# Kernel tuning notes

Measured on AMD Instinct MI355X. Metric: run time of the kernel, lower is better.

The kernel has to match this reference:

```python
import jax, jax.numpy as jnp
import numpy as np

N = 100000      # nodes
E = 1200000     # edges (avg degree ~12)
F_IN = 64       # input feature dim
HID = 64        # hidden_channels
OUT = 64        # out_channels


def setup_inputs() -> dict:
    key = jax.random.key(0)
    ks = jax.random.split(key, 9)
    s_in = 1.0 / np.sqrt(F_IN)
    s_h = 1.0 / np.sqrt(HID)
    inp = {
        "x": jax.random.normal(ks[0], (N, F_IN), dtype=jnp.float32),
        "edge_index": jax.random.randint(ks[1], (2, E), 0, N, dtype=jnp.int64),
        # conv_in: lin_l (with bias) applied to aggregated msgs, lin_r (no bias) to self
        "Wl_in": jax.random.normal(ks[2], (HID, F_IN), dtype=jnp.float32) * s_in,
        "bl_in": jnp.zeros((HID,), dtype=jnp.float32),
        "Wr_in": jax.random.normal(ks[3], (HID, F_IN), dtype=jnp.float32) * s_in,
        # conv_med (shared across the 2 middle applications)
        "Wl_med": jax.random.normal(ks[4], (HID, HID), dtype=jnp.float32) * s_h,
        "bl_med": jnp.zeros((HID,), dtype=jnp.float32),
        "Wr_med": jax.random.normal(ks[5], (HID, HID), dtype=jnp.float32) * s_h,
        # conv_out
        "Wl_out": jax.random.normal(ks[6], (OUT, HID), dtype=jnp.float32) * s_h,
        "bl_out": jnp.zeros((OUT,), dtype=jnp.float32),
        "Wr_out": jax.random.normal(ks[7], (OUT, HID), dtype=jnp.float32) * s_h,
    }
    return inp


def reference(x, edge_index, Wl_in, bl_in, Wr_in, Wl_med, bl_med, Wr_med,
              Wl_out, bl_out, Wr_out):
    src = edge_index[0]
    dst = edge_index[1]
    n = x.shape[0]

    def sage(h, Wl, bl, Wr):
        # sum-aggregate neighbor messages h_j into each destination node i
        agg = jax.ops.segment_sum(h[src], dst, num_segments=n)  # [N, F]
        return agg @ Wl.T + bl + h @ Wr.T

    # eval mode: dropout is identity
    h = jnp.tanh(sage(x, Wl_in, bl_in, Wr_in))
    for _ in range(2):  # conv_med applied twice with shared weights
        h = jnp.tanh(sage(h, Wl_med, bl_med, Wr_med))
    return sage(h, Wl_out, bl_out, Wr_out)
```

## Files before the change

### kernel.cpp

```cpp
#include <hip/hip_runtime.h>
#include <cstdint>

#define F 64
#define TILE1 8192
#define MAXFB 1024
#define SCAN_BLK 1024
#define ECAP 2048

typedef short bf16x8 __attribute__((ext_vector_type(8)));
typedef float f32x4  __attribute__((ext_vector_type(4)));

__device__ __forceinline__ unsigned short f2b(float f) {
    unsigned u = __float_as_uint(f);
    unsigned r = u + 0x7fffu + ((u >> 16) & 1u);
    return (unsigned short)(r >> 16);
}
__device__ __forceinline__ void add8(float* a, uint4 u) {
    const unsigned* p = (const unsigned*)&u;
#pragma unroll
    for (int i = 0; i < 4; ++i) {
        a[2 * i + 0] += __uint_as_float(p[i] << 16);
        a[2 * i + 1] += __uint_as_float(p[i] & 0xffff0000u);
    }
}

__global__ __launch_bounds__(256) void prep_hist_kernel(
    const float* __restrict__ Wl0, const float* __restrict__ Wr0,
    const float* __restrict__ Wl1, const float* __restrict__ Wr1,
    const float* __restrict__ Wl2, const float* __restrict__ Wr2,
    ushort* __restrict__ wbuf,
    const float* __restrict__ x, ushort* __restrict__ xb, int nElem,
    const int* __restrict__ dst, int* __restrict__ binMat,
    int E, int NB1, int nf) {
    __shared__ int h[MAXFB];
    int b = blockIdx.x;
    int t = threadIdx.x;
    if (b < 12) {
        int g = b * 256 + t;
        int set = g >> 10;
        int fl = g & 1023;
        int f = fl >> 6;
        int l = fl & 63;
        int s = f >> 2;
        int ot = f & 3;
        const float* Wl = (set == 0) ? Wl0 : (set == 1) ? Wl1 : Wl2;
        const float* Wr = (set == 0) ? Wr0 : (set == 1) ? Wr1 : Wr2;
        int o = ot * 16 + (l & 15);
        int k0 = s * 32 + (l >> 4) * 8;
        unsigned d[4];
#pragma unroll
        for (int p = 0; p < 4; ++p) {
            int ka = k0 + 2 * p, kb = k0 + 2 * p + 1;
            float va = (ka < 64) ? Wl[o * 64 + ka] : Wr[o * 64 + (ka - 64)];
            float vb = (kb < 64) ? Wl[o * 64 + kb] : Wr[o * 64 + (kb - 64)];
            d[p] = (unsigned)f2b(va) | ((unsigned)f2b(vb) << 16);
        }
        ((uint4*)wbuf)[g] = make_uint4(d[0], d[1], d[2], d[3]);
    } else if (b < 12 + NB1) {
        int tb = b - 12;
        for (int i = t; i < nf; i += 256) h[i] = 0;
        __syncthreads();
        int base = tb * TILE1;
        int end = min(base + TILE1, E);
        const int4* d4 = (const int4*)dst;
        int n4 = (end - base) >> 2;
        int b4 = base >> 2;
        for (int k = t; k < n4; k += 256) {
            int4 v = d4[b4 + k];
            atomicAdd(&h[v.x >> 7], 1);
            atomicAdd(&h[v.y >> 7], 1);
            atomicAdd(&h[v.z >> 7], 1);
            atomicAdd(&h[v.w >> 7], 1);
        }
        __syncthreads();
        for (int i = t; i < nf; i += 256) binMat[i * NB1 + tb] = h[i];
    } else {
        int i = (b - 12 - NB1) * 256 + t;
        int n4 = nElem >> 2;
        if (i < n4) {
            float4 v = ((const float4*)x)[i];
            uint2 o;
            o.x = (unsigned)f2b(v.x) | ((unsigned)f2b(v.y) << 16);
            o.y = (unsigned)f2b(v.z) | ((unsigned)f2b(v.w) << 16);
            ((uint2*)xb)[i] = o;
        }
    }
}

__global__ __launch_bounds__(SCAN_BLK) void scan_blocks_kernel(
    int* __restrict__ a, int* __restrict__ blockSums, int len) {
    __shared__ int sh[SCAN_BLK];
    int t = threadIdx.x;
    int i = blockIdx.x * SCAN_BLK + t;
    int v = (i < len) ? a[i] : 0;
    sh[t] = v;
    __syncthreads();
    for (int off = 1; off < SCAN_BLK; off <<= 1) {
        int add = (t >= off) ? sh[t - off] : 0;
        __syncthreads();
        sh[t] += add;
        __syncthreads();
    }
    int incl = sh[t];
    if (i < len) a[i] = incl - v;
    if (t == SCAN_BLK - 1) blockSums[blockIdx.x] = incl;
}

__device__ __forceinline__ void scan_sums_lds(
    const int* __restrict__ blockSums, int nbScan, int* sBS) {
    int t = threadIdx.x;
    int v = (t < nbScan) ? blockSums[t] : 0;
    sBS[t] = v;
    __syncthreads();
    for (int off = 1; off < 256; off <<= 1) {
        int add = (t >= off) ? sBS[t - off] : 0;
        __syncthreads();
        sBS[t] += add;
        __syncthreads();
    }
    int excl = sBS[t] - v;
    __syncthreads();
    sBS[t] = excl;
    __syncthreads();
}

__global__ __launch_bounds__(256) void scatter_kernel(
    const int* __restrict__ src, const int* __restrict__ dst,
    const int* __restrict__ binMat, const int* __restrict__ blockSums,
    unsigned* __restrict__ stage2, int E, int NB1, int nf, int nbScan) {
    __shared__ int cur[MAXFB];
    __shared__ int sBS[256];
    int t = threadIdx.x;
    scan_sums_lds(blockSums, nbScan, sBS);
    for (int i = t; i < nf; i += 256) {
        int j = i * NB1 + blockIdx.x;
        cur[i] = binMat[j] + sBS[j >> 10];
    }
    __syncthreads();
    int base = blockIdx.x * TILE1;
    int end = min(base + TILE1, E);
    const int4* s4 = (const int4*)src;
    const int4* d4 = (const int4*)dst;
    int n4 = (end - base) >> 2;
    int b4 = base >> 2;
    for (int k = t; k < n4; k += 256) {
        int4 s = s4[b4 + k];
        int4 d = d4[b4 + k];
        int p0 = atomicAdd(&cur[d.x >> 7], 1);
        int p1 = atomicAdd(&cur[d.y >> 7], 1);
        int p2 = atomicAdd(&cur[d.z >> 7], 1);
        int p3 = atomicAdd(&cur[d.w >> 7], 1);
        stage2[p0] = ((unsigned)(d.x & 127) << 17) | (unsigned)s.x;
        stage2[p1] = ((unsigned)(d.y & 127) << 17) | (unsigned)s.y;
        stage2[p2] = ((unsigned)(d.z & 127) << 17) | (unsigned)s.z;
        stage2[p3] = ((unsigned)(d.w & 127) << 17) | (unsigned)s.w;
    }
}

__global__ __launch_bounds__(256) void phase2_kernel(
    const unsigned* __restrict__ stage2, const int* __restrict__ binMat,
    const int* __restrict__ blockSums,
    int* __restrict__ csrSrc, int* __restrict__ rowStart,
    int* __restrict__ perm,
    int E, int NB1, int nf, int nbScan) {
    __shared__ int cnt[128];
    __shared__ int pre[129];
    __shared__ int cur[128];
    __shared__ int sBS[256];
    __shared__ int permL[128];
    int b = blockIdx.x;
    int t = threadIdx.x;
    scan_sums_lds(blockSums, nbScan, sBS);
    int j0 = b * NB1;
    int s = binMat[j0] + sBS[j0 >> 10];
    int e2 = E;
    if (b + 1 < nf) {
        int j1 = (b + 1) * NB1;
        e2 = binMat[j1] + sBS[j1 >> 10];
    }
    if (t < 128) cnt[t] = 0;
    __syncthreads();
    for (int i = s + t; i < e2; i += 256)
        atomicAdd(&cnt[(stage2[i] >> 17) & 127], 1);
    __syncthreads();
    if (t < 128) pre[t + 1] = cnt[t];
    if (t == 0) pre[0] = 0;
    if (t < 128) {
        int my = cnt[t];
        int r = 0;
        for (int j = 0; j < 128; ++j) {
            int cj = cnt[j];
            r += (cj > my) || (cj == my && j < t);
        }
        permL[r] = t;
    }
    __syncthreads();
    for (int off = 1; off < 128; off <<= 1) {
        int v = 0;
        if (t < 128 && (t + 1) > off) v = pre[t + 1 - off];
        __syncthreads();
        if (t < 128 && (t + 1) > off) pre[t + 1] += v;
        __syncthreads();
    }
    if (t < 128) cur[t] = pre[t];
    if (t < 129) rowStart[b * 128 + t] = s + pre[t];
    if (t < 128) perm[b * 128 + t] = permL[t];
    __syncthreads();
    for (int i = s + t; i < e2; i += 256) {
        unsigned w = stage2[i];
        int pos = atomicAdd(&cur[(w >> 17) & 127], 1);
        csrSrc[s + pos] = (int)(w & 0x1FFFFu);
    }
}

__global__ __launch_bounds__(512, 4) void fused_layer(
    const ushort* __restrict__ hb, const int* __restrict__ rowStart,
    const int* __restrict__ csrSrc, const int* __restrict__ perm,
    const ushort* __restrict__ wbuf,
    const float* __restrict__ bl, void* __restrict__ out, int n, int flags) {
    __shared__ __align__(16) ushort smem[128 * 72];
    __shared__ int eidx[ECAP];

    int t = threadIdx.x;
    int node0b = blockIdx.x * 128;
    const uint4* h16 = (const uint4*)hb;

    int e0 = rowStart[node0b];
    int ne = rowStart[node0b + 128] - e0;
    bool useL = (ne <= ECAP);
    if (useL) {
        for (int i = t; i < ne; i += 512) eidx[i] = csrSrc[e0 + i];
    }
    __syncthreads();

    {
        int c = t & 7;
        int tm = t >> 3;
        const int* permB = perm + blockIdx.x * 128;
        int nl0 = permB[tm];
        int nl1 = permB[127 - tm];

        auto run = [&](auto IDX) {
#pragma unroll 1
            for (int r = 0; r < 2; ++r) {
                int nl = (r == 0) ? nl0 : nl1;
                int node = node0b + nl;
                float a[8] = {0.f, 0.f, 0.f, 0.f, 0.f, 0.f, 0.f, 0.f};
                int e = rowStart[node];
                int end = rowStart[node + 1];
                for (; e + 3 < end; e += 4) {
                    int s0 = IDX(e + 0);
                    int s1 = IDX(e + 1);
                    int s2 = IDX(e + 2);
                    int s3 = IDX(e + 3);
                    uint4 u0 = h16[(size_t)s0 * 8 + c];
                    uint4 u1 = h16[(size_t)s1 * 8 + c];
                    uint4 u2 = h16[(size_t)s2 * 8 + c];
                    uint4 u3 = h16[(size_t)s3 * 8 + c];
                    add8(a, u0); add8(a, u1); add8(a, u2); add8(a, u3);
                }
                for (; e < end; ++e) {
                    uint4 u0 = h16[(size_t)IDX(e) * 8 + c];
                    add8(a, u0);
                }
                unsigned d[4];
#pragma unroll
                for (int p = 0; p < 4; ++p)
                    d[p] = (unsigned)f2b(a[2 * p]) | ((unsigned)f2b(a[2 * p + 1]) << 16);
                *(uint4*)(smem + nl * 72 + c * 8) = make_uint4(d[0], d[1], d[2], d[3]);
            }
        };
        if (useL) run([&](int e) { return eidx[e - e0]; });
        else      run([&](int e) { return csrSrc[e]; });
    }
    __syncthreads();

    int w = t >> 6;
    int l = t & 63;
    int quad = l >> 4;
    int lo = l & 15;

    f32x4 acc[4];
#pragma unroll
    for (int ot = 0; ot < 4; ++ot) {
        float bv = bl[ot * 16 + lo];
        f32x4 bvv = {bv, bv, bv, bv};
        acc[ot] = bvv;
    }

#pragma unroll
    for (int s = 0; s < 4; ++s) {
        bf16x8 A;
        if (s < 2) {
            int nl = w * 16 + lo;
            A = *(const bf16x8*)(smem + nl * 72 + s * 32 + quad * 8);
        } else {
            size_t node = (size_t)node0b + w * 16 + lo;
            A = *(const bf16x8*)(hb + node * 64 + (s & 1) * 32 + quad * 8);
        }
#pragma unroll
        for (int ot = 0; ot < 4; ++ot) {
            bf16x8 B = *(const bf16x8*)(wbuf + (((s * 4 + ot) * 64) + l) * 8);
            acc[ot] = __builtin_amdgcn_mfma_f32_16x16x32_bf16(A, B, acc[ot], 0, 0, 0);
        }
    }
    __syncthreads();

    float* outT = (float*)smem;
    int whalf = w >> 2;
    int wrow = (w & 3) * 16;

#pragma unroll
    for (int half = 0; half < 2; ++half) {
        if (whalf == half) {
#pragma unroll
            for (int ot = 0; ot < 4; ++ot) {
                f32x4 v = acc[ot];
                if (flags & 1) {
                    v[0] = tanhf(v[0]); v[1] = tanhf(v[1]);
                    v[2] = tanhf(v[2]); v[3] = tanhf(v[3]);
                }
                int row = wrow + quad * 4;
                int col = ot * 16 + lo;
#pragma unroll
                for (int r = 0; r < 4; ++r)
                    outT[(row + r) * 68 + col] = v[r];
            }
        }
        __syncthreads();
        int hr = t >> 3;
        int node = node0b + half * 64 + hr;
        if (node < n) {
            const float* srcp = &outT[hr * 68 + (t & 7) * 8];
            if (flags & 2) {
                uint4* o8 = (uint4*)out;
                unsigned dd[4];
#pragma unroll
                for (int p = 0; p < 4; ++p) {
                    float va = srcp[2 * p];
                    float vb = srcp[2 * p + 1];
                    dd[p] = (unsigned)f2b(va) | ((unsigned)f2b(vb) << 16);
                }
                o8[(size_t)node * 8 + (t & 7)] = make_uint4(dd[0], dd[1], dd[2], dd[3]);
            } else {
                float4* o16 = (float4*)out;
#pragma unroll
                for (int q = 0; q < 2; ++q) {
                    float4 v = *(const float4*)(srcp + q * 4);
                    o16[(size_t)node * 16 + (t & 7) * 2 + q] = v;
                }
            }
        }
        if (half == 0) __syncthreads();
    }
}

extern "C" void kernel_launch(void* const* d_in, const int* in_sizes, int n_in,
                              void* d_out, int out_size, void* d_ws, size_t ws_size,
                              hipStream_t stream) {
    const float* x      = (const float*)d_in[0];
    const int*   edges  = (const int*)d_in[1];
    const float* Wl_in  = (const float*)d_in[2];
    const float* bl_in  = (const float*)d_in[3];
    const float* Wr_in  = (const float*)d_in[4];
    const float* Wl_med = (const float*)d_in[5];
    const float* bl_med = (const float*)d_in[6];
    const float* Wr_med = (const float*)d_in[7];
    const float* Wl_out = (const float*)d_in[8];
    const float* bl_out = (const float*)d_in[9];
    const float* Wr_out = (const float*)d_in[10];

    const int N = in_sizes[0] / F;
    const int E = in_sizes[1] / 2;
    const int* src = edges;
    const int* dst = edges + E;

    const int nf  = (N + 127) >> 7;
    const int NB1 = (E + TILE1 - 1) / TILE1;
    const int NR  = nf * 128;
    const int scanLen = nf * NB1;
    const int nbScan = (scanLen + SCAN_BLK - 1) / SCAN_BLK;

    ushort*  wbuf      = (ushort*)d_ws;
    ushort*  xb        = wbuf + 3 * 8192;
    ushort*  hAb       = xb + (size_t)NR * F;
    ushort*  hBb       = hAb + (size_t)NR * F;
    int*     rowStart  = (int*)(hBb + (size_t)NR * F);
    int*     blockSums = rowStart + NR + 2;
    int*     binMat    = blockSums + SCAN_BLK;
    unsigned* stage2   = (unsigned*)(binMat + scanLen);
    int*     csrSrc    = (int*)(stage2 + E);
    int*     perm      = csrSrc + E;

    const int prep_blocks = 12 + NB1 + (N * F / 4 + 255) / 256;

    prep_hist_kernel<<<prep_blocks, 256, 0, stream>>>(
        Wl_in, Wr_in, Wl_med, Wr_med, Wl_out, Wr_out, wbuf, x, xb, N * F,
        dst, binMat, E, NB1, nf);
    scan_blocks_kernel<<<nbScan, SCAN_BLK, 0, stream>>>(binMat, blockSums, scanLen);
    scatter_kernel<<<NB1, 256, 0, stream>>>(src, dst, binMat, blockSums, stage2, E, NB1, nf, nbScan);
    phase2_kernel<<<nf, 256, 0, stream>>>(stage2, binMat, blockSums, csrSrc, rowStart, perm, E, NB1, nf, nbScan);

    fused_layer<<<nf, 512, 0, stream>>>(xb,  rowStart, csrSrc, perm, wbuf,         bl_in,  hAb,   N, 3);
    fused_layer<<<nf, 512, 0, stream>>>(hAb, rowStart, csrSrc, perm, wbuf + 8192,  bl_med, hBb,   N, 3);
    fused_layer<<<nf, 512, 0, stream>>>(hBb, rowStart, csrSrc, perm, wbuf + 8192,  bl_med, hAb,   N, 3);
    fused_layer<<<nf, 512, 0, stream>>>(hAb, rowStart, csrSrc, perm, wbuf + 16384, bl_out, d_out, N, 0);
}
```

Baseline: 256.9 us.

## Use 1024-thread blocks: one node per thread group, split MFMA output tiles across waves

The fused SAGE layer kernel now launches 1024 threads per block instead of 512. Each 8-thread group gathers exactly one node rather than two, and the node-to-group mapping uses a strided rank over the degree-sorted permutation to spread load across waves. In the matmul stage, 16 waves each compute two of the four output column tiles, and the store phase uses 16 threads per row. This aims for more memory-level parallelism in the gather, at the cost of fewer resident blocks per CU and more per-block synchronisation.

```diff
diff --git a/kernel.cpp b/kernel.cpp
--- a/kernel.cpp
+++ b/kernel.cpp
@@ -213,7 +213,7 @@
     }
 }
 
-__global__ __launch_bounds__(512, 4) void fused_layer(
+__global__ __launch_bounds__(1024, 2) void fused_layer(
     const ushort* __restrict__ hb, const int* __restrict__ rowStart,
     const int* __restrict__ csrSrc, const int* __restrict__ perm,
     const ushort* __restrict__ wbuf,
@@ -229,126 +229,118 @@
     int ne = rowStart[node0b + 128] - e0;
     bool useL = (ne <= ECAP);
     if (useL) {
-        for (int i = t; i < ne; i += 512) eidx[i] = csrSrc[e0 + i];
+        for (int i = t; i < ne; i += 1024) eidx[i] = csrSrc[e0 + i];
     }
     __syncthreads();
 
     {
         int c = t & 7;
         int tm = t >> 3;
-        const int* permB = perm + blockIdx.x * 128;
-        int nl0 = permB[tm];
-        int nl1 = permB[127 - tm];
+        int rank = ((tm & 7) << 4) + (tm >> 3);
+        int nl = perm[blockIdx.x * 128 + rank];
+        int node = node0b + nl;
+        float a[8] = {0.f, 0.f, 0.f, 0.f, 0.f, 0.f, 0.f, 0.f};
+        int e = rowStart[node];
+        int end = rowStart[node + 1];
 
         auto run = [&](auto IDX) {
-#pragma unroll 1
-            for (int r = 0; r < 2; ++r) {
-                int nl = (r == 0) ? nl0 : nl1;
-                int node = node0b + nl;
-                float a[8] = {0.f, 0.f, 0.f, 0.f, 0.f, 0.f, 0.f, 0.f};
-                int e = rowStart[node];
-                int end = rowStart[node + 1];
-                for (; e + 3 < end; e += 4) {
-                    int s0 = IDX(e + 0);
-                    int s1 = IDX(e + 1);
-                    int s2 = IDX(e + 2);
-                    int s3 = IDX(e + 3);
-                    uint4 u0 = h16[(size_t)s0 * 8 + c];
-                    uint4 u1 = h16[(size_t)s1 * 8 + c];
-                    uint4 u2 = h16[(size_t)s2 * 8 + c];
-                    uint4 u3 = h16[(size_t)s3 * 8 + c];
-                    add8(a, u0); add8(a, u1); add8(a, u2); add8(a, u3);
-                }
-                for (; e < end; ++e) {
-                    uint4 u0 = h16[(size_t)IDX(e) * 8 + c];
-                    add8(a, u0);
-                }
-                unsigned d[4];
-#pragma unroll
-                for (int p = 0; p < 4; ++p)
-                    d[p] = (unsigned)f2b(a[2 * p]) | ((unsigned)f2b(a[2 * p + 1]) << 16);
-                *(uint4*)(smem + nl * 72 + c * 8) = make_uint4(d[0], d[1], d[2], d[3]);
+            for (; e + 3 < end; e += 4) {
+                int s0 = IDX(e + 0);
+                int s1 = IDX(e + 1);
+                int s2 = IDX(e + 2);
+                int s3 = IDX(e + 3);
+                uint4 u0 = h16[(size_t)s0 * 8 + c];
+                uint4 u1 = h16[(size_t)s1 * 8 + c];
+                uint4 u2 = h16[(size_t)s2 * 8 + c];
+                uint4 u3 = h16[(size_t)s3 * 8 + c];
+                add8(a, u0); add8(a, u1); add8(a, u2); add8(a, u3);
+            }
+            for (; e < end; ++e) {
+                uint4 u0 = h16[(size_t)IDX(e) * 8 + c];
+                add8(a, u0);
             }
         };
-        if (useL) run([&](int e) { return eidx[e - e0]; });
-        else      run([&](int e) { return csrSrc[e]; });
+        if (useL) run([&](int ei) { return eidx[ei - e0]; });
+        else      run([&](int ei) { return csrSrc[ei]; });
+
+        unsigned d[4];
+#pragma unroll
+        for (int p = 0; p < 4; ++p)
+            d[p] = (unsigned)f2b(a[2 * p]) | ((unsigned)f2b(a[2 * p + 1]) << 16);
+        *(uint4*)(smem + nl * 72 + c * 8) = make_uint4(d[0], d[1], d[2], d[3]);
     }
     __syncthreads();
 
     int w = t >> 6;
+    int m = w & 7;
+    int oth = w >> 3;
     int l = t & 63;
     int quad = l >> 4;
     int lo = l & 15;
 
-    f32x4 acc[4];
-#pragma unroll
-    for (int ot = 0; ot < 4; ++ot) {
-        float bv = bl[ot * 16 + lo];
+    f32x4 acc[2];
+#pragma unroll
+    for (int oi = 0; oi < 2; ++oi) {
+        float bv = bl[(oth * 2 + oi) * 16 + lo];
         f32x4 bvv = {bv, bv, bv, bv};
-        acc[ot] = bvv;
+        acc[oi] = bvv;
     }
 
 #pragma unroll
     for (int s = 0; s < 4; ++s) {
         bf16x8 A;
         if (s < 2) {
-            int nl = w * 16 + lo;
+            int nl = m * 16 + lo;
             A = *(const bf16x8*)(smem + nl * 72 + s * 32 + quad * 8);
         } else {
-            size_t node = (size_t)node0b + w * 16 + lo;
+            size_t node = (size_t)node0b + m * 16 + lo;
             A = *(const bf16x8*)(hb + node * 64 + (s & 1) * 32 + quad * 8);
         }
 #pragma unroll
-        for (int ot = 0; ot < 4; ++ot) {
+        for (int oi = 0; oi < 2; ++oi) {
+            int ot = oth * 2 + oi;
             bf16x8 B = *(const bf16x8*)(wbuf + (((s * 4 + ot) * 64) + l) * 8);
-            acc[ot] = __builtin_amdgcn_mfma_f32_16x16x32_bf16(A, B, acc[ot], 0, 0, 0);
+            acc[oi] = __builtin_amdgcn_mfma_f32_16x16x32_bf16(A, B, acc[oi], 0, 0, 0);
         }
     }
     __syncthreads();
 
     float* outT = (float*)smem;
-    int whalf = w >> 2;
-    int wrow = (w & 3) * 16;
+    int whalf = m >> 2;
+    int wrow = (m & 3) * 16;
 
 #pragma unroll
     for (int half = 0; half < 2; ++half) {
         if (whalf == half) {
 #pragma unroll
-            for (int ot = 0; ot < 4; ++ot) {
-                f32x4 v = acc[ot];
+            for (int oi = 0; oi < 2; ++oi) {
+                f32x4 v = acc[oi];
                 if (flags & 1) {
                     v[0] = tanhf(v[0]); v[1] = tanhf(v[1]);
                     v[2] = tanhf(v[2]); v[3] = tanhf(v[3]);
                 }
                 int row = wrow + quad * 4;
-                int col = ot * 16 + lo;
+                int col = (oth * 2 + oi) * 16 + lo;
 #pragma unroll
                 for (int r = 0; r < 4; ++r)
                     outT[(row + r) * 68 + col] = v[r];
             }
         }
         __syncthreads();
-        int hr = t >> 3;
+        int hr = t >> 4;
+        int c16 = t & 15;
         int node = node0b + half * 64 + hr;
         if (node < n) {
-            const float* srcp = &outT[hr * 68 + (t & 7) * 8];
+            const float* srcp = &outT[hr * 68 + c16 * 4];
             if (flags & 2) {
-                uint4* o8 = (uint4*)out;
-                unsigned dd[4];
-#pragma unroll
-                for (int p = 0; p < 4; ++p) {
-                    float va = srcp[2 * p];
-                    float vb = srcp[2 * p + 1];
-                    dd[p] = (unsigned)f2b(va) | ((unsigned)f2b(vb) << 16);
-                }
-                o8[(size_t)node * 8 + (t & 7)] = make_uint4(dd[0], dd[1], dd[2], dd[3]);
+                uint2* o4 = (uint2*)out;
+                uint2 dd;
+                dd.x = (unsigned)f2b(srcp[0]) | ((unsigned)f2b(srcp[1]) << 16);
+                dd.y = (unsigned)f2b(srcp[2]) | ((unsigned)f2b(srcp[3]) << 16);
+                o4[(size_t)node * 16 + c16] = dd;
             } else {
                 float4* o16 = (float4*)out;
-#pragma unroll
-                for (int q = 0; q < 2; ++q) {
-                    float4 v = *(const float4*)(srcp + q * 4);
-                    o16[(size_t)node * 16 + (t & 7) * 2 + q] = v;
-                }
+                o16[(size_t)node * 16 + c16] = *(const float4*)srcp;
             }
         }
         if (half == 0) __syncthreads();
@@ -401,8 +393,8 @@
     scatter_kernel<<<NB1, 256, 0, stream>>>(src, dst, binMat, blockSums, stage2, E, NB1, nf, nbScan);
     phase2_kernel<<<nf, 256, 0, stream>>>(stage2, binMat, blockSums, csrSrc, rowStart, perm, E, NB1, nf, nbScan);
 
-    fused_layer<<<nf, 512, 0, stream>>>(xb,  rowStart, csrSrc, perm, wbuf,         bl_in,  hAb,   N, 3);
-    fused_layer<<<nf, 512, 0, stream>>>(hAb, rowStart, csrSrc, perm, wbuf + 8192,  bl_med, hBb,   N, 3);
-    fused_layer<<<nf, 512, 0, stream>>>(hBb, rowStart, csrSrc, perm, wbuf + 8192,  bl_med, hAb,   N, 3);
-    fused_layer<<<nf, 512, 0, stream>>>(hAb, rowStart, csrSrc, perm, wbuf + 16384, bl_out, d_out, N, 0);
-}
+    fused_layer<<<nf, 1024, 0, stream>>>(xb,  rowStart, csrSrc, perm, wbuf,         bl_in,  hAb,   N, 3);
+    fused_layer<<<nf, 1024, 0, stream>>>(hAb, rowStart, csrSrc, perm, wbuf + 8192,  bl_med, hBb,   N, 3);
+    fused_layer<<<nf, 1024, 0, stream>>>(hBb, rowStart, csrSrc, perm, wbuf + 8192,  bl_med, hAb,   N, 3);
+    fused_layer<<<nf, 1024, 0, stream>>>(hAb, rowStart, csrSrc, perm, wbuf + 16384, bl_out, d_out, N, 0);
+}
```

Measured after the change: 278.2 us. 8.3% more time.

## Fuse CSR-building preprocessing kernels into one cooperative kernel with grid syncs

Applied to the files above, without the earlier changes.

Replaces the four separate preprocessing launches (histogram/convert, block scan, scatter, per-bucket sort) with a single cooperative kernel of 256 blocks x 1024 threads that uses grid.sync between phases. The goal is to remove kernel launch gaps and tail effects between the small CSR-construction stages. In exchange, the fixed grid is smaller than the original per-stage grids, so each stage loops over its tiles with fewer parallel blocks. Grid-wide barriers also add their own cost. If the cooperative launch fails, the code falls back to the original four-kernel path.

```diff
diff --git a/kernel.cpp b/kernel.cpp
--- a/kernel.cpp
+++ b/kernel.cpp
@@ -1,11 +1,16 @@
 #include <hip/hip_runtime.h>
+#include <hip/hip_cooperative_groups.h>
 #include <cstdint>
+
+namespace cg = cooperative_groups;
 
 #define F 64
 #define TILE1 8192
 #define MAXFB 1024
 #define SCAN_BLK 1024
 #define ECAP 2048
+#define PRE_BLOCKS 256
+#define PRE_THREADS 1024
 
 typedef short bf16x8 __attribute__((ext_vector_type(8)));
 typedef float f32x4  __attribute__((ext_vector_type(4)));
@@ -21,6 +26,197 @@
     for (int i = 0; i < 4; ++i) {
         a[2 * i + 0] += __uint_as_float(p[i] << 16);
         a[2 * i + 1] += __uint_as_float(p[i] & 0xffff0000u);
+    }
+}
+
+__device__ __forceinline__ void pack_weight_frag(
+    int g, const float* Wl0, const float* Wr0, const float* Wl1,
+    const float* Wr1, const float* Wl2, const float* Wr2, ushort* wbuf) {
+    int set = g >> 10;
+    int fl = g & 1023;
+    int f = fl >> 6;
+    int l = fl & 63;
+    int s = f >> 2;
+    int ot = f & 3;
+    const float* Wl = (set == 0) ? Wl0 : (set == 1) ? Wl1 : Wl2;
+    const float* Wr = (set == 0) ? Wr0 : (set == 1) ? Wr1 : Wr2;
+    int o = ot * 16 + (l & 15);
+    int k0 = s * 32 + (l >> 4) * 8;
+    unsigned d[4];
+#pragma unroll
+    for (int p = 0; p < 4; ++p) {
+        int ka = k0 + 2 * p, kb = k0 + 2 * p + 1;
+        float va = (ka < 64) ? Wl[o * 64 + ka] : Wr[o * 64 + (ka - 64)];
+        float vb = (kb < 64) ? Wl[o * 64 + kb] : Wr[o * 64 + (kb - 64)];
+        d[p] = (unsigned)f2b(va) | ((unsigned)f2b(vb) << 16);
+    }
+    ((uint4*)wbuf)[g] = make_uint4(d[0], d[1], d[2], d[3]);
+}
+
+__global__ __launch_bounds__(PRE_THREADS, 4) void pre_coop(
+    const float* __restrict__ Wl0, const float* __restrict__ Wr0,
+    const float* __restrict__ Wl1, const float* __restrict__ Wr1,
+    const float* __restrict__ Wl2, const float* __restrict__ Wr2,
+    ushort* __restrict__ wbuf,
+    const float* __restrict__ x, ushort* __restrict__ xb, int nElem,
+    const int* __restrict__ src, const int* __restrict__ dst,
+    int* __restrict__ binMat, int* __restrict__ blockSums,
+    unsigned* __restrict__ stage2, int* __restrict__ csrSrc,
+    int* __restrict__ rowStart, int* __restrict__ perm,
+    int E, int NB1, int nf, int scanLen, int nbScan) {
+    cg::grid_group grid = cg::this_grid();
+    __shared__ int shmem[PRE_THREADS];
+
+    const int t = threadIdx.x;
+    const int b = blockIdx.x;
+    const int gid = b * PRE_THREADS + t;
+    const int GT = PRE_BLOCKS * PRE_THREADS;
+
+    if (gid < 3072) pack_weight_frag(gid, Wl0, Wr0, Wl1, Wr1, Wl2, Wr2, wbuf);
+
+    {
+        int n4 = nElem >> 2;
+        const float4* x4 = (const float4*)x;
+        for (int i = gid; i < n4; i += GT) {
+            float4 v = x4[i];
+            uint2 o;
+            o.x = (unsigned)f2b(v.x) | ((unsigned)f2b(v.y) << 16);
+            o.y = (unsigned)f2b(v.z) | ((unsigned)f2b(v.w) << 16);
+            ((uint2*)xb)[i] = o;
+        }
+    }
+    for (int tb = b; tb < NB1; tb += gridDim.x) {
+        for (int i = t; i < nf; i += PRE_THREADS) shmem[i] = 0;
+        __syncthreads();
+        int base = tb * TILE1;
+        int end = min(base + TILE1, E);
+        const int4* d4 = (const int4*)dst;
+        int n4 = (end - base) >> 2;
+        int b4 = base >> 2;
+        for (int k = t; k < n4; k += PRE_THREADS) {
+            int4 v = d4[b4 + k];
+            atomicAdd(&shmem[v.x >> 7], 1);
+            atomicAdd(&shmem[v.y >> 7], 1);
+            atomicAdd(&shmem[v.z >> 7], 1);
+            atomicAdd(&shmem[v.w >> 7], 1);
+        }
+        __syncthreads();
+        for (int i = t; i < nf; i += PRE_THREADS) binMat[i * NB1 + tb] = shmem[i];
+        __syncthreads();
+    }
+    __threadfence();
+    grid.sync();
+
+    {
+        int i = b * PRE_THREADS + t;
+        int v = (b < nbScan && i < scanLen) ? binMat[i] : 0;
+        shmem[t] = v;
+        __syncthreads();
+        for (int off = 1; off < PRE_THREADS; off <<= 1) {
+            int add = (t >= off) ? shmem[t - off] : 0;
+            __syncthreads();
+            shmem[t] += add;
+            __syncthreads();
+        }
+        int incl = shmem[t];
+        if (b < nbScan && i < scanLen) binMat[i] = incl - v;
+        if (b < nbScan && t == PRE_THREADS - 1) blockSums[b] = incl;
+    }
+    __threadfence();
+    grid.sync();
+
+    if (b == 0) {
+        int v = (t < nbScan) ? blockSums[t] : 0;
+        shmem[t] = v;
+        __syncthreads();
+        for (int off = 1; off < PRE_THREADS; off <<= 1) {
+            int add = (t >= off) ? shmem[t - off] : 0;
+            __syncthreads();
+            shmem[t] += add;
+            __syncthreads();
+        }
+        if (t < nbScan) blockSums[t] = shmem[t] - v;
+    }
+    __threadfence();
+    grid.sync();
+
+    for (int tb = b; tb < NB1; tb += gridDim.x) {
+        for (int i = t; i < nf; i += PRE_THREADS) {
+            int j = i * NB1 + tb;
+            shmem[i] = binMat[j] + blockSums[j >> 10];
+        }
+        __syncthreads();
+        int base = tb * TILE1;
+        int end = min(base + TILE1, E);
+        const int4* s4 = (const int4*)src;
+        const int4* d4 = (const int4*)dst;
+        int n4 = (end - base) >> 2;
+        int b4 = base >> 2;
+        for (int k = t; k < n4; k += PRE_THREADS) {
+            int4 s = s4[b4 + k];
+            int4 d = d4[b4 + k];
+            int p0 = atomicAdd(&shmem[d.x >> 7], 1);
+            int p1 = atomicAdd(&shmem[d.y >> 7], 1);
+            int p2 = atomicAdd(&shmem[d.z >> 7], 1);
+            int p3 = atomicAdd(&shmem[d.w >> 7], 1);
+            stage2[p0] = ((unsigned)(d.x & 127) << 17) | (unsigned)s.x;
+            stage2[p1] = ((unsigned)(d.y & 127) << 17) | (unsigned)s.y;
+            stage2[p2] = ((unsigned)(d.z & 127) << 17) | (unsigned)s.z;
+            stage2[p3] = ((unsigned)(d.w & 127) << 17) | (unsigned)s.w;
+        }
+        __syncthreads();
+    }
+    __threadfence();
+    grid.sync();
+
+    {
+        int* cnt   = shmem;
+        int* pre   = shmem + 128;
+        int* curb  = shmem + 272;
+        int* permL = shmem + 416;
+        for (int bk = b; bk < nf; bk += gridDim.x) {
+            int j0 = bk * NB1;
+            int s = binMat[j0] + blockSums[j0 >> 10];
+            int e2 = E;
+            if (bk + 1 < nf) {
+                int j1 = (bk + 1) * NB1;
+                e2 = binMat[j1] + blockSums[j1 >> 10];
+            }
+            if (t < 128) cnt[t] = 0;
+            __syncthreads();
+            for (int i = s + t; i < e2; i += PRE_THREADS)
+                atomicAdd(&cnt[(stage2[i] >> 17) & 127], 1);
+            __syncthreads();
+            if (t < 128) pre[t + 1] = cnt[t];
+            if (t == 0) pre[0] = 0;
+            if (t < 128) {
+                int my = cnt[t];
+                int r = 0;
+                for (int j = 0; j < 128; ++j) {
+                    int cj = cnt[j];
+                    r += (cj > my) || (cj == my && j < t);
+                }
+                permL[r] = t;
+            }
+            __syncthreads();
+            for (int off = 1; off < 128; off <<= 1) {
+                int v = 0;
+                if (t < 128 && (t + 1) > off) v = pre[t + 1 - off];
+                __syncthreads();
+                if (t < 128 && (t + 1) > off) pre[t + 1] += v;
+                __syncthreads();
+            }
+            if (t < 128) curb[t] = pre[t];
+            if (t < 129) rowStart[bk * 128 + t] = s + pre[t];
+            if (t < 128) perm[bk * 128 + t] = permL[t];
+            __syncthreads();
+            for (int i = s + t; i < e2; i += PRE_THREADS) {
+                unsigned w = stage2[i];
+                int pos = atomicAdd(&curb[(w >> 17) & 127], 1);
+                csrSrc[s + pos] = (int)(w & 0x1FFFFu);
+            }
+            __syncthreads();
+        }
     }
 }
 
@@ -36,26 +232,7 @@
     int b = blockIdx.x;
     int t = threadIdx.x;
     if (b < 12) {
-        int g = b * 256 + t;
-        int set = g >> 10;
-        int fl = g & 1023;
-        int f = fl >> 6;
-        int l = fl & 63;
-        int s = f >> 2;
-        int ot = f & 3;
-        const float* Wl = (set == 0) ? Wl0 : (set == 1) ? Wl1 : Wl2;
-        const float* Wr = (set == 0) ? Wr0 : (set == 1) ? Wr1 : Wr2;
-        int o = ot * 16 + (l & 15);
-        int k0 = s * 32 + (l >> 4) * 8;
-        unsigned d[4];
-#pragma unroll
-        for (int p = 0; p < 4; ++p) {
-            int ka = k0 + 2 * p, kb = k0 + 2 * p + 1;
-            float va = (ka < 64) ? Wl[o * 64 + ka] : Wr[o * 64 + (ka - 64)];
-            float vb = (kb < 64) ? Wl[o * 64 + kb] : Wr[o * 64 + (kb - 64)];
-            d[p] = (unsigned)f2b(va) | ((unsigned)f2b(vb) << 16);
-        }
-        ((uint4*)wbuf)[g] = make_uint4(d[0], d[1], d[2], d[3]);
+        pack_weight_frag(b * 256 + t, Wl0, Wr0, Wl1, Wr1, Wl2, Wr2, wbuf);
     } else if (b < 12 + NB1) {
         int tb = b - 12;
         for (int i = t; i < nf; i += 256) h[i] = 0;
@@ -372,8 +549,8 @@
 
     const int N = in_sizes[0] / F;
     const int E = in_sizes[1] / 2;
-    const int* src = edges;
-    const int* dst = edges + E;
+    const int* srcp = edges;
+    const int* dstp = edges + E;
 
     const int nf  = (N + 127) >> 7;
     const int NB1 = (E + TILE1 - 1) / TILE1;
@@ -392,14 +569,30 @@
     int*     csrSrc    = (int*)(stage2 + E);
     int*     perm      = csrSrc + E;
 
-    const int prep_blocks = 12 + NB1 + (N * F / 4 + 255) / 256;
-
-    prep_hist_kernel<<<prep_blocks, 256, 0, stream>>>(
-        Wl_in, Wr_in, Wl_med, Wr_med, Wl_out, Wr_out, wbuf, x, xb, N * F,
-        dst, binMat, E, NB1, nf);
-    scan_blocks_kernel<<<nbScan, SCAN_BLK, 0, stream>>>(binMat, blockSums, scanLen);
-    scatter_kernel<<<NB1, 256, 0, stream>>>(src, dst, binMat, blockSums, stage2, E, NB1, nf, nbScan);
-    phase2_kernel<<<nf, 256, 0, stream>>>(stage2, binMat, blockSums, csrSrc, rowStart, perm, E, NB1, nf, nbScan);
+    int nElem = N * F;
+    int Ei = E, NB1i = NB1, nfi = nf, sLi = scanLen, nbSi = nbScan;
+
+    void* argsP[] = {
+        (void*)&Wl_in, (void*)&Wr_in, (void*)&Wl_med, (void*)&Wr_med,
+        (void*)&Wl_out, (void*)&Wr_out, (void*)&wbuf,
+        (void*)&x, (void*)&xb, (void*)&nElem,
+        (void*)&srcp, (void*)&dstp,
+        (void*)&binMat, (void*)&blockSums, (void*)&stage2,
+        (void*)&csrSrc, (void*)&rowStart, (void*)&perm,
+        (void*)&Ei, (void*)&NB1i, (void*)&nfi, (void*)&sLi, (void*)&nbSi,
+    };
+    hipError_t cerr = hipLaunchCooperativeKernel(
+        pre_coop, dim3(PRE_BLOCKS), dim3(PRE_THREADS), argsP, 0u, stream);
+
+    if (cerr != hipSuccess) {
+        const int prep_blocks = 12 + NB1 + (N * F / 4 + 255) / 256;
+        prep_hist_kernel<<<prep_blocks, 256, 0, stream>>>(
+            Wl_in, Wr_in, Wl_med, Wr_med, Wl_out, Wr_out, wbuf, x, xb, N * F,
+            dstp, binMat, E, NB1, nf);
+        scan_blocks_kernel<<<nbScan, SCAN_BLK, 0, stream>>>(binMat, blockSums, scanLen);
+        scatter_kernel<<<NB1, 256, 0, stream>>>(srcp, dstp, binMat, blockSums, stage2, E, NB1, nf, nbScan);
+        phase2_kernel<<<nf, 256, 0, stream>>>(stage2, binMat, blockSums, csrSrc, rowStart, perm, E, NB1, nf, nbScan);
+    }
 
     fused_layer<<<nf, 512, 0, stream>>>(xb,  rowStart, csrSrc, perm, wbuf,         bl_in,  hAb,   N, 3);
     fused_layer<<<nf, 512, 0, stream>>>(hAb, rowStart, csrSrc, perm, wbuf + 8192,  bl_med, hBb,   N, 3);
```

After: 736.9 us. +186.9%, slower.
